# Kernel optimization log

Measured on AMD Instinct MI355X. Metric: run time of the kernel, lower is better.

The kernel has to match this reference:

```python
import jax, jax.numpy as jnp
import numpy as np

ROI = 9
GROUPS = 32

def _gn(x, gamma, beta, eps):
    B, C, H, W = x.shape
    xr = x.reshape(B, GROUPS, C // GROUPS, H, W)
    m = xr.mean(axis=(2, 3, 4), keepdims=True)
    v = xr.var(axis=(2, 3, 4), keepdims=True)
    xr = (xr - m) / jnp.sqrt(v + eps)
    x = xr.reshape(B, C, H, W)
    if gamma is not None:
        x = x * gamma[None, :, None, None] + beta[None, :, None, None]
    return x

def _conv(x, w, b, pad):
    y = jax.lax.conv_general_dilated(x, w, (1, 1), [(pad, pad), (pad, pad)],
                                     dimension_numbers=('NCHW', 'OIHW', 'NCHW'))
    return y + b[None, :, None, None]

def _roi_align(feat, boxes):
    # torchvision roi_align, spatial_scale=1, aligned=False (roi size clamped to >=1),
    # adaptive sampling ratio -> 1 sample/bin for sub-pixel normalized boxes.
    B, C, H, W = feat.shape
    x1, y1, x2, y2 = boxes[:, 0], boxes[:, 1], boxes[:, 2], boxes[:, 3]
    rw = jnp.maximum(x2 - x1, 1.0)
    rh = jnp.maximum(y2 - y1, 1.0)
    ctr = (jnp.arange(ROI, dtype=feat.dtype) + 0.5) / ROI
    xs = x1[:, None] + ctr[None, :] * rw[:, None]  # [B,ROI]
    ys = y1[:, None] + ctr[None, :] * rh[:, None]
    def samp(img, ysr, xsr):
        yc = jnp.clip(ysr, 0.0, H - 1.0)
        xc = jnp.clip(xsr, 0.0, W - 1.0)
        y0 = jnp.floor(yc).astype(jnp.int32)
        x0 = jnp.floor(xc).astype(jnp.int32)
        y1i = jnp.minimum(y0 + 1, H - 1)
        x1i = jnp.minimum(x0 + 1, W - 1)
        ly = yc - y0
        lx = xc - x0
        v00 = img[:, y0[:, None], x0[None, :]]
        v01 = img[:, y0[:, None], x1i[None, :]]
        v10 = img[:, y1i[:, None], x0[None, :]]
        v11 = img[:, y1i[:, None], x1i[None, :]]
        w00 = (1 - ly)[:, None] * (1 - lx)[None, :]
        w01 = (1 - ly)[:, None] * lx[None, :]
        w10 = ly[:, None] * (1 - lx)[None, :]
        w11 = ly[:, None] * lx[None, :]
        return v00 * w00 + v01 * w01 + v10 * w10 + v11 * w11
    return jax.vmap(samp)(feat, ys, xs)

def _paste(global_x, x_local, bbox):
    # per-box nearest interpolate of 9x9 patch to (y2-y1, x2-x1) and additive scatter,
    # expressed as a dense gather over the full HxW grid (jit-friendly).
    B, C, H, W = global_x.shape
    bb = jnp.floor(bbox * H).astype(jnp.int32)  # bbox >= 0 so trunc == floor
    x1b, y1b = bb[:, 0], bb[:, 1]
    x2b = jnp.maximum(bb[:, 2], x1b + 1)
    y2b = jnp.maximum(bb[:, 3], y1b + 1)
    r = jnp.arange(H)
    jy = r[None, :] - y1b[:, None]
    jx = r[None, :] - x1b[:, None]
    oh = (y2b - y1b)[:, None]
    ow = (x2b - x1b)[:, None]
    sy = jnp.clip((jy * ROI) // oh, 0, ROI - 1)  # F.interpolate 'nearest': floor(j*in/out)
    sx = jnp.clip((jx * ROI) // ow, 0, ROI - 1)
    iny = (jy >= 0) & (r[None, :] < y2b[:, None])
    inx = (jx >= 0) & (r[None, :] < x2b[:, None])
    m = iny[:, :, None] & inx[:, None, :]  # [B,H,W]
    def one(xi, syi, sxi, mi):
        return jnp.where(mi[None], xi[:, syi][:, :, sxi], 0.0)
    return global_x + jax.vmap(one)(x_local, sy, sx, m)

def reference(global_x, context, indicator, bbox, cond_flag,
              ln_g, ln_b, cn_g, cn_b, Wq, bq, Wk, bk, Wv, bv, Wsg, bsg, Wsb, bsb):
    B, C, H, W = global_x.shape
    T, D = context.shape[1], context.shape[2]
    Hc = 16
    ctx_map = jnp.transpose(context, (0, 2, 1)).reshape(B, D, Hc, Hc)
    ctx_mean = jnp.mean(context, axis=1, keepdims=True)              # [B,1,D]
    mean_map = jnp.transpose(ctx_mean, (0, 2, 1))[:, :, :, None]     # [B,D,1,1]
    ctx_map = jnp.where(cond_flag[:, None, None, None], ctx_map, mean_map)
    ctx = jnp.where(cond_flag[:, None, None], context, ctx_mean)
    x = _roi_align(global_x, bbox)                                   # [B,C,9,9]
    x = _gn(x, ln_g, ln_b, 1e-6)
    ind = jnp.broadcast_to(indicator[:, :, None, None], (B, indicator.shape[1], ROI, ROI))
    x = jnp.concatenate([x, ind], axis=1)
    q = _conv(x, Wq, bq, 0).reshape(B, C, ROI * ROI).transpose(0, 2, 1)        # [B,81,C]
    k = _conv(_gn(ctx_map, cn_g, cn_b, 1e-6), Wk, bk, 0).reshape(B, C, T).transpose(0, 2, 1)
    v = _conv(ctx_map, Wv, bv, 1).reshape(B, C, T).transpose(0, 2, 1)
    attn = jax.nn.softmax(jnp.einsum('bic,bjc->bij', q, k), axis=-1)  # no scale (as in source)
    xa = jnp.einsum('bij,bjc->bic', attn, v).transpose(0, 2, 1).reshape(B, C, ROI, ROI)
    ac = jnp.einsum('bij,bjd->bid', attn, ctx).transpose(0, 2, 1).reshape(B, D, ROI, ROI)
    x = _gn(xa, None, None, 1e-5) * _conv(ac, Wsg, bsg, 1) + _conv(ac, Wsb, bsb, 1)  # SPADE
    out = _paste(global_x, x, bbox)
    return (out, attn)

def setup_inputs():
    key = jax.random.key(0)
    ks = jax.random.split(key, 12)
    B, C, H, D, T = 32, 320, 64, 1024, 256
    s = 0.02
    global_x = jax.random.normal(ks[0], (B, C, H, H), jnp.float32)
    context = jax.random.normal(ks[1], (B, T, D), jnp.float32)
    indicator = (jax.random.uniform(ks[2], (B, 2)) > 0.5).astype(jnp.float32)
    c0 = jax.random.uniform(ks[3], (B, 2), minval=0.05, maxval=0.5)
    wh = jax.random.uniform(ks[4], (B, 2), minval=0.15, maxval=0.45)
    bbox = jnp.concatenate([c0, jnp.minimum(c0 + wh, 1.0)], axis=1)
    cond_flag = jax.random.randint(ks[5], (B,), 0, 2) > 0
    return {
        'global_x': global_x, 'context': context, 'indicator': indicator,
        'bbox': bbox, 'cond_flag': cond_flag,
        'ln_g': jnp.ones((C,)), 'ln_b': jnp.zeros((C,)),
        'cn_g': jnp.ones((D,)), 'cn_b': jnp.zeros((D,)),
        'Wq': jax.random.normal(ks[6], (C, C + 2, 1, 1)) * s, 'bq': jnp.zeros((C,)),
        'Wk': jax.random.normal(ks[7], (C, D, 1, 1)) * s, 'bk': jnp.zeros((C,)),
        'Wv': jax.random.normal(ks[8], (C, D, 3, 3)) * s, 'bv': jnp.zeros((C,)),
        'Wsg': jax.random.normal(ks[9], (C, D, 3, 3)) * s, 'bsg': jnp.zeros((C,)),
        'Wsb': jax.random.normal(ks[10], (C, D, 3, 3)) * s, 'bsb': jnp.zeros((C,)),
    }
```

## Files before the change

kernel.cpp:

```cpp
#include <hip/hip_runtime.h>
#include <hip/hip_bf16.h>

#define DINLINE __device__ __forceinline__

typedef short short8 __attribute__((ext_vector_type(8)));
typedef float f32x4 __attribute__((ext_vector_type(4)));
typedef unsigned short u16;

DINLINE u16 f2b(float f) {
  __hip_bfloat16 h = __float2bfloat16(f);
  return *reinterpret_cast<u16*>(&h);
}
DINLINE float b2f(u16 u) {
  __hip_bfloat16 h = *reinterpret_cast<__hip_bfloat16*>(&u);
  return __bfloat162float(h);
}

DINLINE void gload16(const u16* g, u16* l) {
  __builtin_amdgcn_global_load_lds((const __attribute__((address_space(1))) void*)g,
                                   (__attribute__((address_space(3))) void*)l, 16, 0, 0);
}

DINLINE void wave_red2(float& s, float& s2) {
  for (int o = 32; o > 0; o >>= 1) { s += __shfl_down(s, o); s2 += __shfl_down(s2, o); }
}


struct RowA {
  const u16* A; int physW;
  struct RS { const u16* base; };
  DINLINE RS row(long p) const { return { A + p * (long)physW }; }
  DINLINE const u16* ptr(const RS& rs, int kk) const { return rs.base + (kk << 6); }
};
struct TriA {
  const u16* A; int physW; int nhi;
  struct RS { const u16* base; };
  DINLINE RS row(long p) const { return { A + p * (long)physW }; }
  DINLINE const u16* ptr(const RS& rs, int kk) const {
    int c = (int)(((unsigned)kk * 171u) >> 9), r = kk - 3 * c;
    return rs.base + (((r == 1 ? nhi : 0) + c) << 6);
  }
};
struct ShiftVA {
  const u16* src; const u16* zp;
  struct RS { int y, x; const u16* bbase; };
  DINLINE RS row(long p) const {
    int b = (int)(p >> 8), ps = (int)p & 255;
    return { ps >> 4, ps & 15, src + ((long)b << 18) };
  }
  DINLINE const u16* ptr(const RS& rs, int kk) const {
    int c = (int)(((unsigned)kk * 57u) >> 9), s = kk - 9 * c;
    int sy = (s * 11) >> 5, sx = s - sy * 3;
    int yy = rs.y + sy - 1, xx = rs.x + sx - 1;
    bool ok = ((unsigned)yy < 16u) & ((unsigned)xx < 16u);
    return ok ? rs.bbase + (((yy << 4) + xx) << 10) + (c << 6) : zp;
  }
};
struct Shift9A {
  const u16* src; const u16* zp;
  struct RS { int y, x; const u16* bbase; int pin; };
  DINLINE RS row(long p) const {
    int pi = (int)p;
    int b = pi / 81, pp = pi - b * 81;
    int pin = pi < 2592 ? 1 : 0;
    if (b > 31) b = 31;
    return { pp / 9, pp % 9, src + ((long)b << 17), pin };
  }
  DINLINE const u16* ptr(const RS& rs, int kk) const {
    int c = (int)(((unsigned)kk * 57u) >> 9), s = kk - 9 * c;
    int sy = (s * 11) >> 5, sx = s - sy * 3;
    int yy = rs.y + sy - 1, xx = rs.x + sx - 1;
    bool ok = rs.pin && ((unsigned)yy < 9u) && ((unsigned)xx < 9u);
    return ok ? rs.bbase + ((yy * 9 + xx) << 10) + (c << 6) : zp;
  }
};


struct RowB {
  const u16* B; int physW; long bstride;
  struct RS { const u16* base; };
  DINLINE RS row(int by, long j) const { return { B + ((long)(by >> 1) * bstride + j) * physW }; }
  DINLINE const u16* ptr(const RS& rs, int kk) const { return rs.base + (kk << 6); }
};
struct TriB {
  const u16* B; int physW; int nhi; long bstride;
  struct RS { const u16* base; };
  DINLINE RS row(int by, long j) const { return { B + ((long)(by >> 1) * bstride + j) * physW }; }
  DINLINE const u16* ptr(const RS& rs, int kk) const {
    int c = (int)(((unsigned)kk * 171u) >> 9), r = kk - 3 * c;
    return rs.base + (((r == 2 ? nhi : 0) + c) << 6);
  }
};
struct ShiftWB {
  const u16* W;
  struct RS { const u16* base; };
  DINLINE RS row(int, long j) const { return { W + j * 9216 }; }
  DINLINE const u16* ptr(const RS& rs, int kk) const {
    int c = (int)(((unsigned)kk * 57u) >> 9), s = kk - 9 * c;
    return rs.base + (s << 10) + (c << 6);
  }
};


struct EpiHiLo {
  u16* o; const float* bias;
  DINLINE void operator()(long p, int j, float v) const {
    v += bias[j];
    u16 hi = f2b(v), lo = f2b(v - b2f(hi));
    u16* q = o + p * 640 + j;
    q[0] = hi; q[320] = lo;
  }
};
struct EpiHiLoP {
  u16* o; const float* bias;
  DINLINE void operator()(int, long p, int j, float v) const {
    if (j >= 320) return;
    v += bias[j];
    u16 hi = f2b(v), lo = f2b(v - b2f(hi));
    u16* q = o + p * 640 + j;
    q[0] = hi; q[320] = lo;
  }
};
struct EpiLog {
  float* attn;
  DINLINE void operator()(long p, int j, float v) const {
    int b = (int)(p >> 7), i = (int)p & 127;
    if (i < 81) attn[((long)b * 81 + i) * 256 + j] = v;
  }
};
struct EpiXaAc {
  float* xa; u16* ac;
  DINLINE void operator()(long p, int j, float v) const {
    int b = (int)(p >> 7), i = (int)p & 127;
    if (j < 320) {
      xa[((long)b * 128 + i) * 320 + j] = v;
    } else {
      ac[((long)b * 128 + i) * 1024 + (j - 320)] = f2b(v);
    }
  }
};
struct EpiPart {
  float* buf; long pstride; int jw;
  DINLINE void operator()(int part, long p, int j, float v) const {
    buf[(long)part * pstride + p * (long)jw + j] = v;
  }
};


template <class AS, class BS, class EPI>
DINLINE void gemm_pipe_body(u16* lds, AS a, BS bsrc, int gy, int nch, EPI epi,
                            int subN, int bid) {
  const int q = subN >> 3, r8 = subN & 7;
  const int j8 = bid & 7, pos = bid >> 3;
  const int lid = (j8 < r8) ? j8 * (q + 1) + pos : r8 * (q + 1) + (j8 - r8) * q + pos;
  const int by = lid % gy, bx = lid / gy;

  const int tid = threadIdx.x;
  const int w = tid >> 6, lane = tid & 63;
  const int wm = w >> 1, wn = w & 1;
  const long p0 = (long)by * 64;
  const int j0 = bx * 64;

  const int r0 = tid >> 3;
  const int csw = (((lane & 7) ^ (lane >> 3)) << 3);
  auto rsA0 = a.row(p0 + r0);
  auto rsA1 = a.row(p0 + r0 + 32);
  auto rsB0 = bsrc.row(by, j0 + r0);
  auto rsB1 = bsrc.row(by, j0 + r0 + 32);
  u16* lA0 = lds + w * 512;
  u16* lA1 = lds + 2048 + w * 512;
  u16* lB0 = lds + 8192 + w * 512;
  u16* lB1 = lds + 8192 + 2048 + w * 512;

  f32x4 acc[2][2];
#pragma unroll
  for (int x = 0; x < 2; ++x)
#pragma unroll
    for (int y = 0; y < 2; ++y) acc[x][y] = (f32x4){0.f, 0.f, 0.f, 0.f};

  const int fr = lane & 15, fs = lane >> 4, fx = lane & 7;
  const int arow0 = (wm * 32 + fr) * 64;
  const int brow0 = (wn * 32 + fr) * 64;

  gload16(a.ptr(rsA0, 0) + csw, lA0);
  gload16(a.ptr(rsA1, 0) + csw, lA1);
  gload16(bsrc.ptr(rsB0, 0) + csw, lB0);
  gload16(bsrc.ptr(rsB1, 0) + csw, lB1);

  for (int kk = 0; kk < nch; ++kk) {
    const int cur = kk & 1;
    if (kk + 1 < nch) {
      const int nxt = cur ^ 1;
      gload16(a.ptr(rsA0, kk + 1) + csw, lA0 + nxt * 4096);
      gload16(a.ptr(rsA1, kk + 1) + csw, lA1 + nxt * 4096);
      gload16(bsrc.ptr(rsB0, kk + 1) + csw, lB0 + nxt * 4096);
      gload16(bsrc.ptr(rsB1, kk + 1) + csw, lB1 + nxt * 4096);
      asm volatile("s_waitcnt vmcnt(4)" ::: "memory");
    } else {
      asm volatile("s_waitcnt vmcnt(0)" ::: "memory");
    }
    __builtin_amdgcn_s_barrier();
    __builtin_amdgcn_sched_barrier(0);
    short8 af[2][2], bf[2][2];
#pragma unroll
    for (int fm = 0; fm < 2; ++fm)
#pragma unroll
      for (int kh = 0; kh < 2; ++kh) {
        int slot = ((((kh << 2) | fs) ^ fx) << 3);
        af[fm][kh] = *(const short8*)(lds + cur * 4096 + arow0 + fm * 1024 + slot);
      }
#pragma unroll
    for (int fn = 0; fn < 2; ++fn)
#pragma unroll
      for (int kh = 0; kh < 2; ++kh) {
        int slot = ((((kh << 2) | fs) ^ fx) << 3);
        bf[fn][kh] = *(const short8*)(lds + 8192 + cur * 4096 + brow0 + fn * 1024 + slot);
      }
#pragma unroll
    for (int kh = 0; kh < 2; ++kh)
#pragma unroll
      for (int fm = 0; fm < 2; ++fm)
#pragma unroll
        for (int fn = 0; fn < 2; ++fn)
          acc[fm][fn] = __builtin_amdgcn_mfma_f32_16x16x32_bf16(af[fm][kh], bf[fn][kh], acc[fm][fn], 0, 0, 0);
    __builtin_amdgcn_sched_barrier(0);
    __builtin_amdgcn_s_barrier();
  }

  const long ip = p0 + wm * 32 + fs * 4;
  const int jb = j0 + wn * 32 + fr;
#pragma unroll
  for (int fm = 0; fm < 2; ++fm)
#pragma unroll
    for (int fn = 0; fn < 2; ++fn)
#pragma unroll
      for (int rr = 0; rr < 4; ++rr)
        epi(ip + fm * 16 + rr, jb + fn * 16, acc[fm][fn][rr]);
}


template <int NF, class AS, class BS, class EPI>
DINLINE void gemm128_body(u16* lds, AS a, BS bsrc, int gy, int gp, int nchw, EPI epi,
                          int subN, int bid, int j0base) {
  const int q = subN >> 3, r8 = subN & 7;
  const int j8 = bid & 7, pos = bid >> 3;
  const int lid = (j8 < r8) ? j8 * (q + 1) + pos : r8 * (q + 1) + (j8 - r8) * q + pos;
  const int gyp = gy * gp;
  const int bx = lid / gyp;
  const int rem = lid - bx * gyp;
  const int by = rem % gy;
  const int part = rem / gy;
  const int k0 = part * nchw;

  const int tid = threadIdx.x;
  const int w = tid >> 6, lane = tid & 63;
  const int wm = w >> 1, wn = w & 1;
  const long p0 = (long)by * 128;
  const int j0 = j0base + bx * (NF * 32);

  const int r0 = tid >> 3;
  const int csw = (((lane & 7) ^ (lane >> 3)) << 3);
  typename AS::RS rsA[4];
  typename BS::RS rsB[NF];
#pragma unroll
  for (int i = 0; i < 4; ++i) rsA[i] = a.row(p0 + r0 + 32 * i);
#pragma unroll
  for (int i = 0; i < NF; ++i) rsB[i] = bsrc.row(by, (long)j0 + r0 + 32 * i);

  f32x4 acc[4][NF];
#pragma unroll
  for (int x = 0; x < 4; ++x)
#pragma unroll
    for (int y = 0; y < NF; ++y) acc[x][y] = (f32x4){0.f, 0.f, 0.f, 0.f};

  const int fr = lane & 15, fs = lane >> 4, fx = lane & 7;

  for (int kk = 0; kk < nchw; ++kk) {
    __syncthreads();
#pragma unroll
    for (int i = 0; i < 4; ++i)
      gload16(a.ptr(rsA[i], k0 + kk) + csw, lds + (i * 32 + w * 8) * 64);
#pragma unroll
    for (int i = 0; i < NF; ++i)
      gload16(bsrc.ptr(rsB[i], k0 + kk) + csw, lds + 8192 + (i * 32 + w * 8) * 64);
    __syncthreads();
#pragma unroll
    for (int kh = 0; kh < 2; ++kh) {
      const int slot = ((((kh << 2) | fs) ^ fx) << 3);
      short8 af[4], bf[NF];
#pragma unroll
      for (int i = 0; i < 4; ++i)
        af[i] = *(const short8*)(lds + (wm * 64 + i * 16 + fr) * 64 + slot);
#pragma unroll
      for (int i = 0; i < NF; ++i)
        bf[i] = *(const short8*)(lds + 8192 + (wn * (NF * 16) + i * 16 + fr) * 64 + slot);
#pragma unroll
      for (int fm = 0; fm < 4; ++fm)
#pragma unroll
        for (int fn = 0; fn < NF; ++fn)
          acc[fm][fn] = __builtin_amdgcn_mfma_f32_16x16x32_bf16(af[fm], bf[fn], acc[fm][fn], 0, 0, 0);
    }
  }

  const long ip = p0 + wm * 64 + fs * 4;
  const int jb = j0 + wn * (NF * 16) + fr;
#pragma unroll
  for (int fm = 0; fm < 4; ++fm)
#pragma unroll
    for (int fn = 0; fn < NF; ++fn)
#pragma unroll
      for (int rr = 0; rr < 4; ++rr)
        epi(part, ip + fm * 16 + rr, jb + fn * 16, acc[fm][fn][rr]);
}

__global__ void k_prep0(const float* __restrict__ ctx, const int* __restrict__ cond,
                        const float* __restrict__ gx, const float* __restrict__ bbox,
                        const float* __restrict__ Wk, const float* __restrict__ Wq,
                        const float* __restrict__ Wv, const float* __restrict__ Wsg,
                        const float* __restrict__ Wsb,
                        float* __restrict__ cmean, float* __restrict__ stats,
                        float* __restrict__ roix, u16* __restrict__ oK, u16* __restrict__ oQ,
                        u16* __restrict__ Wv_r, u16* __restrict__ Wsgsb) {
  __shared__ float shf[4][2];
  __shared__ float cp[8][32];
  __shared__ float cm32[32];
  __shared__ int iy0[9], iy1[9], ix0[9], ix1[9];
  __shared__ float fly[9], flx[9];
  __shared__ u16 l[9216];
  int bid = blockIdx.x;
  int tid = threadIdx.x;

  if (bid < 1024) {
    int b = bid >> 5, g = bid & 31;
    const float* src = ctx + (size_t)b * 262144 + g * 32;
    int c = tid & 31, tg = tid >> 5;
    float cs = 0.f, s = 0.f, s2 = 0.f;
#pragma unroll 4
    for (int k = 0; k < 32; ++k) {
      int t = tg + k * 8;
      float v = src[(size_t)t * 1024 + c];
      cs += v; s += v; s2 += v * v;
    }
    cp[tg][c] = cs;
    wave_red2(s, s2);
    int lane = tid & 63, w = tid >> 6;
    if (lane == 0) { shf[w][0] = s; shf[w][1] = s2; }
    __syncthreads();
    if (tid < 32) {
      float colsum = 0.f;
#pragma unroll
      for (int k = 0; k < 8; ++k) colsum += cp[k][tid];
      float mv = colsum * (1.f / 256.f);
      cmean[b * 1024 + g * 32 + tid] = mv;
      cm32[tid] = mv;
    }
    __syncthreads();
    if (tid == 0) {
      float m, var;
      if (cond[b]) {
        float ts = shf[0][0] + shf[1][0] + shf[2][0] + shf[3][0];
        float ts2 = shf[0][1] + shf[1][1] + shf[2][1] + shf[3][1];
        m = ts * (1.f / 8192.f);
        var = ts2 * (1.f / 8192.f) - m * m;
      } else {
        float ms = 0.f, ms2 = 0.f;
#pragma unroll
        for (int k = 0; k < 32; ++k) { ms += cm32[k]; ms2 += cm32[k] * cm32[k]; }
        m = ms * (1.f / 32.f);
        var = ms2 * (1.f / 32.f) - m * m;
      }
      stats[bid * 2] = m;
      stats[bid * 2 + 1] = 1.f / sqrtf(var + 1e-6f);
    }
    return;
  }
  if (bid < 1056) {
    int b = bid - 1024;
    int t = tid;
    if (t < 9) {
      float x1 = bbox[b * 4 + 0], y1 = bbox[b * 4 + 1], x2 = bbox[b * 4 + 2], y2 = bbox[b * 4 + 3];
      float rw = fmaxf(x2 - x1, 1.f), rh = fmaxf(y2 - y1, 1.f);
      float ctr = ((float)t + 0.5f) / 9.0f;
      float yc = fminf(fmaxf(y1 + ctr * rh, 0.f), 63.f);
      int y0 = (int)floorf(yc);
      iy0[t] = y0; iy1[t] = min(y0 + 1, 63); fly[t] = yc - (float)y0;
      float xc = fminf(fmaxf(x1 + ctr * rw, 0.f), 63.f);
      int x0 = (int)floorf(xc);
      ix0[t] = x0; ix1[t] = min(x0 + 1, 63); flx[t] = xc - (float)x0;
    }
    __syncthreads();
    for (int idx = t; idx < 320 * 81; idx += 256) {
      int c = idx / 81, p = idx - c * 81;
      int py = p / 9, px = p - py * 9;
      const float* img = gx + ((size_t)b * 320 + c) * 4096;
      float ly = fly[py], lx = flx[px];
      float v00 = img[iy0[py] * 64 + ix0[px]];
      float v01 = img[iy0[py] * 64 + ix1[px]];
      float v10 = img[iy1[py] * 64 + ix0[px]];
      float v11 = img[iy1[py] * 64 + ix1[px]];
      roix[((size_t)b * 320 + c) * 81 + p] =
          v00 * (1.f - ly) * (1.f - lx) + v01 * (1.f - ly) * lx + v10 * ly * (1.f - lx) + v11 * ly * lx;
    }
    return;
  }
  int bid2 = bid - 1056;
  if (bid2 < 1536) {
    int i = bid2 * 256 + tid;
    int c = i >> 10, d = i & 1023;
    float v = (i < 327680) ? Wk[i] : 0.f;
    u16 hi = f2b(v), lo = f2b(v - b2f(hi));
    u16* p = oK + (size_t)c * 2048 + d;
    p[0] = hi; p[1024] = lo;
    return;
  }
  if (bid2 < 2016) {
    int i = (bid2 - 1536) * 256 + tid;
    if (i >= 122880) return;
    int c = i / 384, k = i - c * 384;
    float v = (k < 322) ? Wq[c * 322 + k] : 0.f;
    u16 hi = f2b(v), lo = f2b(v - b2f(hi));
    u16* p = oQ + (size_t)c * 768 + k;
    p[0] = hi; p[384] = lo;
    return;
  }
  int cc = bid2 - 2016;
  const float* src = nullptr; u16* dst;
  if (cc < 384) { dst = Wv_r + (size_t)cc * 9216; if (cc < 320) src = Wv + (size_t)cc * 9216; }
  else if (cc < 704) { src = Wsg + (size_t)(cc - 384) * 9216; dst = Wsgsb + (size_t)(cc - 384) * 9216; }
  else { src = Wsb + (size_t)(cc - 704) * 9216; dst = Wsgsb + (size_t)(320 + cc - 704) * 9216; }
  if (src == nullptr) {
    for (int i = tid; i < 9216; i += 256) dst[i] = 0;
    return;
  }
  for (int i = tid; i < 9216; i += 256) l[i] = f2b(src[i]);
  __syncthreads();
  for (int i = tid; i < 9216; i += 256) {
    int r = i >> 10, d = i & 1023;
    dst[i] = l[d * 9 + r];
  }
}

__global__ __launch_bounds__(256) void k_prep1(
    const float* __restrict__ ctx, const float* __restrict__ cmean,
    const float* __restrict__ st, const float* __restrict__ cng,
    const float* __restrict__ cnb, const int* __restrict__ cond,
    u16* __restrict__ sel, u16* __restrict__ bvc, u16* __restrict__ cn2,
    const float* __restrict__ roix, float* __restrict__ lnst) {
  __shared__ u16 tile[64][66];
  __shared__ float sh[4][2];
  int bid = blockIdx.x;
  if (bid < 2048) {
    int b = bid >> 6;
    int d0 = ((bid >> 2) & 15) * 64;
    int t0 = (bid & 3) * 64;
    bool cf = cond[b] != 0;
#pragma unroll
    for (int q = 0; q < 16; ++q) {
      int idx = q * 256 + threadIdx.x;
      int r = idx >> 6, c = idx & 63;
      int t = t0 + r, d = d0 + c;
      float v = cf ? ctx[((size_t)b * 256 + t) * 1024 + d] : cmean[b * 1024 + d];
      u16 sv = f2b(v);
      sel[((size_t)b * 256 + t) * 1024 + d] = sv;
      tile[r][c] = sv;
      int gi = (b << 5) + (d >> 5);
      float nv = (v - st[gi * 2]) * st[gi * 2 + 1] * cng[d] + cnb[d];
      u16 hi = f2b(nv);
      u16 lo = f2b(nv - b2f(hi));
      size_t rbase = ((size_t)b * 256 + t) * 2048;
      cn2[rbase + d] = hi;
      cn2[rbase + 1024 + d] = lo;
    }
    __syncthreads();
#pragma unroll
    for (int q = 0; q < 16; ++q) {
      int idx = q * 256 + threadIdx.x;
      int r = idx >> 6, c = idx & 63;
      bvc[((size_t)b * 1344 + 320 + d0 + r) * 256 + t0 + c] = tile[c][r];
    }
    return;
  }
  int bg = bid - 2048;
  const float* p = roix + (size_t)bg * 810;
  float s = 0.f, s2 = 0.f;
  for (int i = threadIdx.x; i < 810; i += 256) { float v = p[i]; s += v; s2 += v * v; }
  wave_red2(s, s2);
  int lane = threadIdx.x & 63, w = threadIdx.x >> 6;
  if (lane == 0) { sh[w][0] = s; sh[w][1] = s2; }
  __syncthreads();
  if (threadIdx.x == 0) {
    s = sh[0][0] + sh[1][0] + sh[2][0] + sh[3][0];
    s2 = sh[0][1] + sh[1][1] + sh[2][1] + sh[3][1];
    float m = s * (1.f / 810.f);
    float var = s2 * (1.f / 810.f) - m * m;
    lnst[bg * 2] = m;
    lnst[bg * 2 + 1] = 1.f / sqrtf(var + 1e-6f);
  }
}

__global__ void k_aq2(const float* __restrict__ roix, const float* __restrict__ st,
                      const float* __restrict__ lng, const float* __restrict__ lnb,
                      const float* __restrict__ ind, u16* __restrict__ o) {
  int i = blockIdx.x * 256 + threadIdx.x;
  if (i >= 32 * 128 * 384) return;
  int b = i / (128 * 384), rem = i - b * (128 * 384);
  int row = rem / 384, k = rem - row * 384;
  float v = 0.f;
  if (row < 81) {
    if (k < 320) {
      float x = roix[((size_t)b * 320 + k) * 81 + row];
      int gi = (b << 5) + k / 10;
      v = (x - st[gi * 2]) * st[gi * 2 + 1] * lng[k] + lnb[k];
    } else if (k < 322) v = ind[b * 2 + (k - 320)];
  }
  u16 hi = f2b(v);
  u16 lo = f2b(v - b2f(hi));
  u16* p = o + ((size_t)b * 128 + row) * 768 + k;
  p[0] = hi; p[384] = lo;
}

__global__ __launch_bounds__(256, 3) void k_gemms(
    const u16* __restrict__ cn2, const u16* __restrict__ Wk2, u16* __restrict__ k2,
    const float* __restrict__ bk,
    const u16* __restrict__ sel, const u16* __restrict__ Wv_r, const u16* __restrict__ zpage,
    float* __restrict__ partV,
    const u16* __restrict__ Aq2, const u16* __restrict__ Wq2, u16* __restrict__ q2,
    const float* __restrict__ bq) {
  __shared__ u16 lds[16384];
  int bid = blockIdx.x;
  if (bid < 128) {
    gemm128_body<4>(lds, TriA{cn2, 2048, 16}, TriB{Wk2, 2048, 16, 0}, 64, 1, 48,
                    EpiHiLoP{k2, bk}, 128, bid, 0);
  } else if (bid < 192) {
    gemm128_body<2>(lds, TriA{cn2, 2048, 16}, TriB{Wk2, 2048, 16, 0}, 64, 1, 48,
                    EpiHiLoP{k2, bk}, 64, bid - 128, 256);
  } else if (bid < 448) {
    gemm128_body<4>(lds, ShiftVA{sel, zpage}, ShiftWB{Wv_r}, 64, 2, 72,
                    EpiPart{partV, (long)8192 * 384, 384}, 256, bid - 192, 0);
  } else if (bid < 576) {
    gemm128_body<2>(lds, ShiftVA{sel, zpage}, ShiftWB{Wv_r}, 64, 2, 72,
                    EpiPart{partV, (long)8192 * 384, 384}, 128, bid - 448, 256);
  } else {
    gemm_pipe_body(lds, TriA{Aq2, 768, 6}, TriB{Wq2, 768, 6, 0}, 64, 18,
                   EpiHiLo{q2, bq}, 320, bid - 576);
  }
}

__global__ __launch_bounds__(256, 4) void k_mid(
    const float* __restrict__ partV, const float* __restrict__ bv, u16* __restrict__ bvc,
    const u16* __restrict__ q2, const u16* __restrict__ k2, float* __restrict__ attn) {
  __shared__ u16 lds[16384];
  int bid = blockIdx.x;
  if (bid < 640) {
    int b = bid / 20, rem = bid - b * 20;
    int t0 = (rem & 3) * 64, j0 = (rem >> 2) * 64;
    const long pstride = (long)8192 * 384;
#pragma unroll
    for (int q = 0; q < 16; ++q) {
      int idx = q * 256 + threadIdx.x;
      int r = idx >> 6, c = idx & 63;
      long p = (long)b * 256 + t0 + r;
      const float* src = partV + p * 384 + j0 + c;
      float v = src[0] + src[pstride] + bv[j0 + c];
      lds[r * 66 + c] = f2b(v);
    }
    __syncthreads();
#pragma unroll
    for (int q = 0; q < 16; ++q) {
      int idx = q * 256 + threadIdx.x;
      int r = idx >> 6, c = idx & 63;
      bvc[((long)b * 1344 + j0 + r) * 256 + t0 + c] = lds[c * 66 + r];
    }
    return;
  }
  gemm_pipe_body(lds, TriA{q2, 640, 5}, TriB{k2, 640, 5, 256}, 64, 15,
                 EpiLog{attn}, 256, bid - 640);
}

__global__ void k_softmax2(float* __restrict__ attn, u16* __restrict__ attn_bf) {
  int i = blockIdx.x, b = blockIdx.y;
  int t = threadIdx.x;
  if (i >= 81) { attn_bf[((size_t)b * 128 + i) * 256 + t] = 0; return; }
  float* p = attn + ((size_t)b * 81 + i) * 256;
  float v = p[t];
  float m = v;
  for (int o = 32; o > 0; o >>= 1) m = fmaxf(m, __shfl_down(m, o));
  __shared__ float sm[4], ss[4];
  if ((t & 63) == 0) sm[t >> 6] = m;
  __syncthreads();
  m = fmaxf(fmaxf(sm[0], sm[1]), fmaxf(sm[2], sm[3]));
  float e = expf(v - m);
  float s = e;
  for (int o = 32; o > 0; o >>= 1) s += __shfl_down(s, o);
  if ((t & 63) == 0) ss[t >> 6] = s;
  __syncthreads();
  s = ss[0] + ss[1] + ss[2] + ss[3];
  float r = e / s;
  p[t] = r;
  attn_bf[((size_t)b * 128 + i) * 256 + t] = f2b(r);
}

template <class AS, class BS, class EPI>
__global__ __launch_bounds__(256, 4) void gemm_pipe(AS a, BS bsrc, int gy, int nch, EPI epi) {
  __shared__ u16 lds[16384];
  gemm_pipe_body(lds, a, bsrc, gy, nch, epi, gridDim.x, blockIdx.x);
}

__global__ __launch_bounds__(256, 3) void k_post(
    const float* __restrict__ xa, float* __restrict__ xast,
    const u16* __restrict__ ac_bf, const u16* __restrict__ zpage,
    const u16* __restrict__ Wsgsb, float* __restrict__ part_f) {
  __shared__ u16 lds[16384];
  int bid = blockIdx.x;
  if (bid < 1024) {
    int b = bid >> 5, g = bid & 31;
    float s = 0.f, s2 = 0.f;
    for (int e = threadIdx.x; e < 810; e += 256) {
      int i = e / 10, cc = e - i * 10;
      float v = xa[((long)b * 128 + i) * 320 + g * 10 + cc];
      s += v; s2 += v * v;
    }
    wave_red2(s, s2);
    float* sh = (float*)lds;
    int lane = threadIdx.x & 63, w = threadIdx.x >> 6;
    if (lane == 0) { sh[w * 2] = s; sh[w * 2 + 1] = s2; }
    __syncthreads();
    if (threadIdx.x == 0) {
      s = sh[0] + sh[2] + sh[4] + sh[6];
      s2 = sh[1] + sh[3] + sh[5] + sh[7];
      float m = s * (1.f / 810.f);
      float var = s2 * (1.f / 810.f) - m * m;
      xast[bid * 2] = m;
      xast[bid * 2 + 1] = 1.f / sqrtf(var + 1e-5f);
    }
    return;
  }
  gemm128_body<4>(lds, Shift9A{ac_bf, zpage}, ShiftWB{Wsgsb}, 21, 4, 36,
                  EpiPart{part_f, (long)2688 * 640, 640}, 420, bid - 1024, 0);
}

__global__ void k_sum_sgsb(const float* __restrict__ buf, long pstride,
                           const float* __restrict__ bsg, const float* __restrict__ bsb,
                           const float* __restrict__ xa, const float* __restrict__ st,
                           float* __restrict__ xl) {
  __shared__ float sgb[640];
  __shared__ float ms[32], rss[32];
  long p = blockIdx.x;
  int b = (int)(p / 81), pp = (int)(p - (long)b * 81);
  const float* src = buf + p * 640;
  for (int j = threadIdx.x; j < 640; j += 256) {
    float v = 0.f;
#pragma unroll
    for (int t = 0; t < 4; ++t) v += src[t * pstride + j];
    sgb[j] = v + (j < 320 ? bsg[j] : bsb[j - 320]);
  }
  if (threadIdx.x < 32) {
    ms[threadIdx.x] = st[(b * 32 + threadIdx.x) * 2];
    rss[threadIdx.x] = st[(b * 32 + threadIdx.x) * 2 + 1];
  }
  __syncthreads();
  for (int c = threadIdx.x; c < 320; c += 256) {
    int g = c / 10;
    float xv = xa[((long)b * 128 + pp) * 320 + c];
    xl[((long)b * 81 + pp) * 320 + c] = (xv - ms[g]) * rss[g] * sgb[c] + sgb[320 + c];
  }
}

__global__ void k_paste(const float* __restrict__ gx, const float* __restrict__ bbox,
                        const float* __restrict__ xl, float* __restrict__ out) {
  int bc = blockIdx.x;
  int b = bc / 320;
  int c = bc - b * 320;
  __shared__ int sy[64], sx[64];
  __shared__ unsigned char my[64], mx[64];
  int x1b = (int)floorf(bbox[b * 4 + 0] * 64.f);
  int y1b = (int)floorf(bbox[b * 4 + 1] * 64.f);
  int x2b = max((int)floorf(bbox[b * 4 + 2] * 64.f), x1b + 1);
  int y2b = max((int)floorf(bbox[b * 4 + 3] * 64.f), y1b + 1);
  int t = threadIdx.x;
  if (t < 64) {
    int jy = t - y1b, oh = y2b - y1b;
    my[t] = (jy >= 0 && t < y2b) ? 1 : 0;
    sy[t] = my[t] ? min(jy * 9 / oh, 8) : 0;
    int jx = t - x1b, ow = x2b - x1b;
    mx[t] = (jx >= 0 && t < x2b) ? 1 : 0;
    sx[t] = mx[t] ? min(jx * 9 / ow, 8) : 0;
  }
  __syncthreads();
  size_t base = (size_t)bc * 4096;
  const float* xlb = xl + ((long)b * 81) * 320 + c;
  const float4* g4 = (const float4*)(gx + base);
  float4* o4 = (float4*)(out + base);
#pragma unroll
  for (int it = 0; it < 4; ++it) {
    int idx = it * 256 + t;
    int y = idx >> 4, x0 = (idx & 15) << 2;
    float4 v = g4[idx];
    if (my[y]) {
      const float* row = xlb + (long)sy[y] * 9 * 320;
      if (mx[x0 + 0]) v.x += row[(long)sx[x0 + 0] * 320];
      if (mx[x0 + 1]) v.y += row[(long)sx[x0 + 1] * 320];
      if (mx[x0 + 2]) v.z += row[(long)sx[x0 + 2] * 320];
      if (mx[x0 + 3]) v.w += row[(long)sx[x0 + 3] * 320];
    }
    o4[idx] = v;
  }
}


extern "C" void kernel_launch(void* const* d_in, const int* in_sizes, int n_in,
                              void* d_out, int out_size, void* d_ws, size_t ws_size,
                              hipStream_t stream) {
  const float* gx   = (const float*)d_in[0];
  const float* ctx  = (const float*)d_in[1];
  const float* ind  = (const float*)d_in[2];
  const float* bbox = (const float*)d_in[3];
  const int*   cond = (const int*)d_in[4];
  const float* ln_g = (const float*)d_in[5];
  const float* ln_b = (const float*)d_in[6];
  const float* cn_g = (const float*)d_in[7];
  const float* cn_b = (const float*)d_in[8];
  const float* Wq = (const float*)d_in[9];   const float* bq = (const float*)d_in[10];
  const float* Wk = (const float*)d_in[11];  const float* bk = (const float*)d_in[12];
  const float* Wv = (const float*)d_in[13];  const float* bv = (const float*)d_in[14];
  const float* Wsg = (const float*)d_in[15]; const float* bsg = (const float*)d_in[16];
  const float* Wsb = (const float*)d_in[17]; const float* bsb = (const float*)d_in[18];

  char* base = (char*)d_out;
  float* out = (float*)d_out;
  float* attn_out = out + (size_t)41943040;

  u16* sel     = (u16*)(base + 0);
  u16* bvc     = (u16*)(base + 16777216);
  u16* cn2     = (u16*)(base + 38797312);
  u16* Aq2     = (u16*)(base + 72351744);
  float* part_f= (float*)(base + 38797312);
  u16* k2      = (u16*)(base + 78643200);
  u16* q2      = (u16*)(base + 89128960);
  u16* attn_bf = (u16*)(base + 94371840);
  u16* ac_bf   = (u16*)(base + 96468992);
  u16* Wk2     = (u16*)(base + 108175360);
  u16* Wq2     = (u16*)(base + 109748224);
  u16* Wv_r    = (u16*)(base + 110239744);
  u16* Wsgsb   = (u16*)(base + 117317632);
  float* partV = (float*)(base + 129114112);
  float* xa_f  = (float*)(base + 154279936);
  u16* zpage   = Wv_r + (size_t)320 * 9216;

  float* cmean = (float*)d_ws;
  float* cnst  = cmean + 32768;
  float* lnst  = cnst + 2048;
  float* xast  = lnst + 2048;
  float* roix  = xast + 2048;
  float* xloc  = roix + 829440;

  k_prep0<<<4096, 256, 0, stream>>>(ctx, cond, gx, bbox, Wk, Wq, Wv, Wsg, Wsb,
                                    cmean, cnst, roix, Wk2, Wq2, Wv_r, Wsgsb);
  k_prep1<<<3072, 256, 0, stream>>>(ctx, cmean, cnst, cn_g, cn_b, cond, sel, bvc, cn2,
                                    roix, lnst);
  k_aq2<<<6144, 256, 0, stream>>>(roix, lnst, ln_g, ln_b, ind, Aq2);

  k_gemms<<<896, 256, 0, stream>>>(cn2, Wk2, k2, bk, sel, Wv_r, zpage, partV,
                                   Aq2, Wq2, q2, bq);
  k_mid<<<896, 256, 0, stream>>>(partV, bv, bvc, q2, k2, attn_out);
  k_softmax2<<<dim3(128, 32), 256, 0, stream>>>(attn_out, attn_bf);
  gemm_pipe<<<1344, 256, 0, stream>>>(RowA{attn_bf, 256}, RowB{bvc, 256, 1344},
                                      64, 4, EpiXaAc{xa_f, ac_bf});
  k_post<<<1444, 256, 0, stream>>>(xa_f, xast, ac_bf, zpage, Wsgsb, part_f);
  k_sum_sgsb<<<2592, 256, 0, stream>>>(part_f, (long)2688 * 640, bsg, bsb, xa_f, xast, xloc);

  k_paste<<<10240, 256, 0, stream>>>(gx, bbox, xloc, out);
}
```

Baseline: 307.9 us.

## Overlap bulk global_x copy into output with earlier GEMM kernels

```diff
diff --git a/kernel.cpp b/kernel.cpp
--- a/kernel.cpp
+++ b/kernel.cpp
@@ -23,6 +23,13 @@
 
 DINLINE void wave_red2(float& s, float& s2) {
   for (int o = 32; o > 0; o >>= 1) { s += __shfl_down(s, o); s2 += __shfl_down(s2, o); }
+}
+
+DINLINE void do_copy(float* out, const float* gx, long f4lo, long f4hi, int cb, int ncb) {
+  const float4* s = (const float4*)gx;
+  float4* d = (float4*)out;
+  for (long i = f4lo + (long)cb * 256 + threadIdx.x; i < f4hi; i += (long)ncb * 256)
+    d[i] = s[i];
 }
 
 
@@ -548,7 +555,8 @@
 
 __global__ __launch_bounds__(256, 4) void k_mid(
     const float* __restrict__ partV, const float* __restrict__ bv, u16* __restrict__ bvc,
-    const u16* __restrict__ q2, const u16* __restrict__ k2, float* __restrict__ attn) {
+    const u16* __restrict__ q2, const u16* __restrict__ k2, float* __restrict__ attn,
+    const float* __restrict__ gx, float* __restrict__ outf) {
   __shared__ u16 lds[16384];
   int bid = blockIdx.x;
   if (bid < 640) {
@@ -573,8 +581,16 @@
     }
     return;
   }
-  gemm_pipe_body(lds, TriA{q2, 640, 5}, TriB{k2, 640, 5, 256}, 64, 15,
-                 EpiLog{attn}, 256, bid - 640);
+  if (bid < 896) {
+    gemm_pipe_body(lds, TriA{q2, 640, 5}, TriB{k2, 640, 5, 256}, 64, 15,
+                   EpiLog{attn}, 256, bid - 640);
+    return;
+  }
+  int cb = bid - 896;
+  do_copy(outf, gx, 0, 1048576, cb, 512);
+  do_copy(outf, gx, 4145152, 4915200, cb, 512);
+  do_copy(outf, gx, 6553600, 7258624, cb, 512);
+  do_copy(outf, gx, 9970176, 10485760, cb, 512);
 }
 
 __global__ void k_softmax2(float* __restrict__ attn, u16* __restrict__ attn_bf) {
@@ -600,16 +616,27 @@
   attn_bf[((size_t)b * 128 + i) * 256 + t] = f2b(r);
 }
 
-template <class AS, class BS, class EPI>
-__global__ __launch_bounds__(256, 4) void gemm_pipe(AS a, BS bsrc, int gy, int nch, EPI epi) {
+__global__ __launch_bounds__(256, 4) void k_attn(
+    const u16* __restrict__ attn_bf, const u16* __restrict__ bvc,
+    float* __restrict__ xa, u16* __restrict__ ac,
+    const float* __restrict__ gx, float* __restrict__ outf) {
   __shared__ u16 lds[16384];
-  gemm_pipe_body(lds, a, bsrc, gy, nch, epi, gridDim.x, blockIdx.x);
+  int bid = blockIdx.x;
+  if (bid < 1344) {
+    gemm_pipe_body(lds, RowA{attn_bf, 256}, RowB{bvc, 256, 1344}, 64, 4,
+                   EpiXaAc{xa, ac}, 1344, bid);
+    return;
+  }
+  int cb = bid - 1344;
+  do_copy(outf, gx, 4915200, 5898240, cb, 512);
+  do_copy(outf, gx, 8069632, 9642496, cb, 512);
 }
 
 __global__ __launch_bounds__(256, 3) void k_post(
     const float* __restrict__ xa, float* __restrict__ xast,
     const u16* __restrict__ ac_bf, const u16* __restrict__ zpage,
-    const u16* __restrict__ Wsgsb, float* __restrict__ part_f) {
+    const u16* __restrict__ Wsgsb, float* __restrict__ part_f,
+    const float* __restrict__ gx, float* __restrict__ outf) {
   __shared__ u16 lds[16384];
   int bid = blockIdx.x;
   if (bid < 1024) {
@@ -635,17 +662,30 @@
     }
     return;
   }
-  gemm128_body<4>(lds, Shift9A{ac_bf, zpage}, ShiftWB{Wsgsb}, 21, 4, 36,
-                  EpiPart{part_f, (long)2688 * 640, 640}, 420, bid - 1024, 0);
+  if (bid < 1444) {
+    gemm128_body<4>(lds, Shift9A{ac_bf, zpage}, ShiftWB{Wsgsb}, 21, 4, 36,
+                    EpiPart{part_f, (long)2688 * 640, 640}, 420, bid - 1024, 0);
+    return;
+  }
+  int cb = bid - 1444;
+  do_copy(outf, gx, 1048576, 2424832, cb, 256);
+  do_copy(outf, gx, 5898240, 6029312, cb, 256);
 }
 
 __global__ void k_sum_sgsb(const float* __restrict__ buf, long pstride,
                            const float* __restrict__ bsg, const float* __restrict__ bsb,
                            const float* __restrict__ xa, const float* __restrict__ st,
-                           float* __restrict__ xl) {
+                           float* __restrict__ xl,
+                           const float* __restrict__ gx, float* __restrict__ outf) {
   __shared__ float sgb[640];
   __shared__ float ms[32], rss[32];
   long p = blockIdx.x;
+  if (p >= 2592) {
+    int cb = (int)p - 2592;
+    do_copy(outf, gx, 6029312, 6553600, cb, 256);
+    do_copy(outf, gx, 7258624, 8069632, cb, 256);
+    return;
+  }
   int b = (int)(p / 81), pp = (int)(p - (long)b * 81);
   const float* src = buf + p * 640;
   for (int j = threadIdx.x; j < 640; j += 256) {
@@ -689,20 +729,42 @@
   __syncthreads();
   size_t base = (size_t)bc * 4096;
   const float* xlb = xl + ((long)b * 81) * 320 + c;
-  const float4* g4 = (const float4*)(gx + base);
   float4* o4 = (float4*)(out + base);
-#pragma unroll
-  for (int it = 0; it < 4; ++it) {
-    int idx = it * 256 + t;
-    int y = idx >> 4, x0 = (idx & 15) << 2;
-    float4 v = g4[idx];
-    if (my[y]) {
-      const float* row = xlb + (long)sy[y] * 9 * 320;
-      if (mx[x0 + 0]) v.x += row[(long)sx[x0 + 0] * 320];
-      if (mx[x0 + 1]) v.y += row[(long)sx[x0 + 1] * 320];
-      if (mx[x0 + 2]) v.z += row[(long)sx[x0 + 2] * 320];
-      if (mx[x0 + 3]) v.w += row[(long)sx[x0 + 3] * 320];
-    }
+  bool typeB = (bc >= 2368 && bc < 4048) || (bc >= 9416 && bc < 9737);
+  if (typeB) {
+    const float4* g4 = (const float4*)(gx + base);
+#pragma unroll
+    for (int it = 0; it < 4; ++it) {
+      int idx = it * 256 + t;
+      int y = idx >> 4, x0 = (idx & 15) << 2;
+      float4 v = g4[idx];
+      if (my[y]) {
+        const float* row = xlb + (long)sy[y] * 9 * 320;
+        if (mx[x0 + 0]) v.x += row[(long)sx[x0 + 0] * 320];
+        if (mx[x0 + 1]) v.y += row[(long)sx[x0 + 1] * 320];
+        if (mx[x0 + 2]) v.z += row[(long)sx[x0 + 2] * 320];
+        if (mx[x0 + 3]) v.w += row[(long)sx[x0 + 3] * 320];
+      }
+      o4[idx] = v;
+    }
+    return;
+  }
+  int yH = min(y2b, 64);
+  int xqL = x1b >> 2;
+  int xqH = min((x2b + 3) >> 2, 16);
+  int nxq = xqH - xqL;
+  int nq = (yH - y1b) * nxq;
+  for (int e = t; e < nq; e += 256) {
+    int ry = y1b + e / nxq;
+    int qx = xqL + (e - (e / nxq) * nxq);
+    int idx = ry * 16 + qx;
+    float4 v = o4[idx];
+    int x0 = qx << 2;
+    const float* row = xlb + (long)sy[ry] * 9 * 320;
+    if (mx[x0 + 0]) v.x += row[(long)sx[x0 + 0] * 320];
+    if (mx[x0 + 1]) v.y += row[(long)sx[x0 + 1] * 320];
+    if (mx[x0 + 2]) v.z += row[(long)sx[x0 + 2] * 320];
+    if (mx[x0 + 3]) v.w += row[(long)sx[x0 + 3] * 320];
     o4[idx] = v;
   }
 }
@@ -762,12 +824,12 @@
 
   k_gemms<<<896, 256, 0, stream>>>(cn2, Wk2, k2, bk, sel, Wv_r, zpage, partV,
                                    Aq2, Wq2, q2, bq);
-  k_mid<<<896, 256, 0, stream>>>(partV, bv, bvc, q2, k2, attn_out);
+  k_mid<<<1408, 256, 0, stream>>>(partV, bv, bvc, q2, k2, attn_out, gx, out);
   k_softmax2<<<dim3(128, 32), 256, 0, stream>>>(attn_out, attn_bf);
-  gemm_pipe<<<1344, 256, 0, stream>>>(RowA{attn_bf, 256}, RowB{bvc, 256, 1344},
-                                      64, 4, EpiXaAc{xa_f, ac_bf});
-  k_post<<<1444, 256, 0, stream>>>(xa_f, xast, ac_bf, zpage, Wsgsb, part_f);
-  k_sum_sgsb<<<2592, 256, 0, stream>>>(part_f, (long)2688 * 640, bsg, bsb, xa_f, xast, xloc);
+  k_attn<<<1856, 256, 0, stream>>>(attn_bf, bvc, xa_f, ac_bf, gx, out);
+  k_post<<<1700, 256, 0, stream>>>(xa_f, xast, ac_bf, zpage, Wsgsb, part_f, gx, out);
+  k_sum_sgsb<<<2848, 256, 0, stream>>>(part_f, (long)2688 * 640, bsg, bsb, xa_f, xast, xloc,
+                                       gx, out);
 
   k_paste<<<10240, 256, 0, stream>>>(gx, bbox, xloc, out);
 }
```

Result: slower. 330.2 us (+7.2%).
